# Kernel optimization log

Hardware: AMD Instinct MI355X
Metric: run time of the kernel (lower is better)

## Reference

```python
import jax, jax.numpy as jnp
import numpy as np

N, E, H = 40000, 640000, 128
EPS = 1e-5

def _bn(x, gamma, beta):
    # BatchNorm1d training-mode forward: batch mean / biased variance over axis 0
    mu = jnp.mean(x, axis=0)
    var = jnp.mean((x - mu) ** 2, axis=0)
    return (x - mu) * jax.lax.rsqrt(var + EPS) * gamma + beta


def setup_inputs() -> dict:
    key = jax.random.key(0)
    ks = jax.random.split(key, 12)
    s = 1.0 / np.sqrt(H)
    return {
        "x_feat": jax.random.normal(ks[0], (N, H), jnp.float32),
        "edge_attr": jax.random.normal(ks[1], (E, H), jnp.float32),
        "bases": jax.random.normal(ks[2], (E, H), jnp.float32),
        "src": jax.random.randint(ks[3], (E,), 0, N, jnp.int32),
        "dst": jax.random.randint(ks[4], (E,), 0, N, jnp.int32),
        "W1": jax.random.uniform(ks[5], (H, H), jnp.float32, -s, s),
        "b1": jnp.zeros((H,), jnp.float32),
        "W2": jax.random.uniform(ks[6], (H, H), jnp.float32, -s, s),
        "b2": jnp.zeros((H,), jnp.float32),
        "g1": jnp.ones((H,), jnp.float32),
        "be1": jnp.zeros((H,), jnp.float32),
        "W3": jax.random.uniform(ks[7], (H, H), jnp.float32, -s, s),
        "b3": jnp.zeros((H,), jnp.float32),
        "g2": jnp.ones((H,), jnp.float32),
        "be2": jnpp_zeros if False else jnp.zeros((H,), jnp.float32),
    }


def reference(x_feat, edge_attr, bases, src, dst,
              W1, b1, W2, b2, g1, be1, W3, b3, g2, be2):
    n_nodes = x_feat.shape[0]
    # edge gather-add: pos_e = x[src] + e
    pos_e = x_feat[src] + edge_attr                       # [E, H]
    # pre_ffn (Linear + exact GELU) then elementwise scale by bases
    v = jax.nn.gelu(pos_e @ W1.T + b1, approximate=False) * bases  # [E, H]
    # scatter-sum aggregation to destination nodes
    aggr = jax.ops.segment_sum(v, dst, num_segments=n_nodes)       # [N, H]
    # ffn: Linear -> BN -> GELU -> Linear -> BN -> GELU
    h = _bn(aggr @ W2.T + b2, g1, be1)
    h = jax.nn.gelu(h, approximate=False)
    h = _bn(h @ W3.T + b3, g2, be2)
    return jax.nn.gelu(h, approximate=False)
```

## Files before the change

### kernel.cpp

```cpp
#include <hip/hip_runtime.h>
#include <cmath>

#define H 128
#define EPS 1e-5f

typedef __attribute__((ext_vector_type(8))) __bf16 bf16x8;
typedef __attribute__((ext_vector_type(4))) float f32x4;
typedef __attribute__((ext_vector_type(2))) float f32x2;
typedef __attribute__((ext_vector_type(4))) unsigned short u16x4;
typedef __attribute__((ext_vector_type(8))) unsigned short u16x8;
typedef __attribute__((ext_vector_type(4))) int i32x4;

__device__ __forceinline__ float gelu_fast(float x) {
    float t2 = -1.5957691216057308f * fmaf(0.044715f * x * x, x, x);
    return x * __builtin_amdgcn_rcpf(1.0f + __expf(t2));
}

__device__ __forceinline__ unsigned short f2bfu(float f) {
    __bf16 h = (__bf16)f;
    return __builtin_bit_cast(unsigned short, h);
}

__device__ __forceinline__ float bfu2f(unsigned short u) {
    return __builtin_bit_cast(float, (unsigned)u << 16);
}

__device__ __forceinline__ void gld16(const void* g, void* l) {
    __builtin_amdgcn_global_load_lds(
        (__attribute__((address_space(1))) void*)(g),
        (__attribute__((address_space(3))) void*)(l), 16, 0, 0);
}

__global__ __launch_bounds__(256) void zero_kernel(int* __restrict__ p, int n4)
{
    int i = blockIdx.x * blockDim.x + threadIdx.x;
    const int stride = gridDim.x * blockDim.x;
    i32x4 z = {0, 0, 0, 0};
    for (; i < n4; i += stride)
        reinterpret_cast<i32x4*>(p)[i] = z;
}

__global__ __launch_bounds__(256) void hist_kernel(const int* __restrict__ dst,
                                                   int* __restrict__ cnt, int E)
{
    int i = blockIdx.x * blockDim.x + threadIdx.x;
    const int stride = gridDim.x * blockDim.x;
    for (; i < E; i += stride) atomicAdd(&cnt[dst[i]], 1);
}

__global__ __launch_bounds__(1024) void scan_kernel(const int* __restrict__ cnt,
                                                    int* __restrict__ offs,
                                                    int Nn, int E)
{
    __shared__ int part[1024];
    const int t = threadIdx.x;
    const int CH = (Nn + 1023) / 1024;
    const int base = t * CH;
    int s = 0;
    for (int i = 0; i < CH; ++i) {
        int idx = base + i;
        if (idx < Nn) s += cnt[idx];
    }
    part[t] = s;
    __syncthreads();
    for (int d = 1; d < 1024; d <<= 1) {
        int v = (t >= d) ? part[t - d] : 0;
        __syncthreads();
        part[t] += v;
        __syncthreads();
    }
    int run = (t > 0) ? part[t - 1] : 0;
    for (int i = 0; i < CH; ++i) {
        int idx = base + i;
        if (idx < Nn) {
            offs[idx] = run;
            run += cnt[idx];
        }
    }
    if (t == 0) offs[Nn] = E;
}

__global__ __launch_bounds__(256) void scatter_perm(const int* __restrict__ dst,
                                                    const int* __restrict__ offs,
                                                    int* __restrict__ cur2,
                                                    int* __restrict__ perm,
                                                    int* __restrict__ dsts, int E)
{
    int i = blockIdx.x * blockDim.x + threadIdx.x;
    const int stride = gridDim.x * blockDim.x;
    for (; i < E; i += stride) {
        int n = dst[i];
        int p = offs[n] + atomicAdd(&cur2[n], 1);
        perm[p] = i;
        dsts[p] = n;
    }
}

__global__ __launch_bounds__(256, 2) void edge_aggr(
    const float* __restrict__ x, const float* __restrict__ ea,
    const float* __restrict__ bases, const int* __restrict__ src,
    const int* __restrict__ perm, const int* __restrict__ dsts,
    const float* __restrict__ W1, const float* __restrict__ b1,
    float* __restrict__ aggr, int E)
{
    __shared__ __align__(16) float ealds[64 * 128];
    __shared__ __align__(16) float blds[64 * 128];
    __shared__ __align__(16) unsigned short xlds[64 * 128];

    const int tid = threadIdx.x;
    const int w = tid >> 6, l = tid & 63, lg = l >> 4, lr = l & 15;

    bf16x8 wf[2][4];
    f32x4 b1v[2];
#pragma unroll
    for (int ni = 0; ni < 2; ++ni) {
        int row = w * 32 + ni * 16 + lr;
#pragma unroll
        for (int kk = 0; kk < 4; ++kk) {
            const float* p = W1 + row * H + kk * 32 + lg * 8;
            u16x8 tt;
#pragma unroll
            for (int i = 0; i < 8; ++i) tt[i] = f2bfu(p[i]);
            wf[ni][kk] = __builtin_bit_cast(bf16x8, tt);
        }
        b1v[ni] = *reinterpret_cast<const f32x4*>(b1 + w * 32 + ni * 16 + lg * 4);
    }

    const int e0 = blockIdx.x * 64;
    int ic = e0 + l;
    ic = ic < E ? ic : E - 1;
    const int el_reg = perm[ic];
    const int nd_reg = dsts[ic];
    const int sr_reg = src[el_reg];

#pragma unroll
    for (int j = 0; j < 8; ++j) {
        const int r = (w << 4) + (j << 1) + (l >> 5);
        const int e = __shfl(el_reg, r);
        const int cs = (l & 31) ^ (r & 7);
        const int rowbase = (((w << 4) + (j << 1)) << 7);
        gld16(ea + (long)e * H + cs * 4, &ealds[rowbase]);
        gld16(bases + (long)e * H + cs * 4, &blds[rowbase]);
    }

#pragma unroll
    for (int it = 0; it < 8; ++it) {
        const int gch = it * 256 + tid;
        const int row = gch >> 5, c16 = gch & 31;
        const int s = __shfl(sr_reg, row);
        f32x4 b = *reinterpret_cast<const f32x4*>(x + (long)s * H + c16 * 4);
        u16x4 o;
#pragma unroll
        for (int j = 0; j < 4; ++j) o[j] = f2bfu(b[j]);
        const int scol = (c16 * 4) ^ ((row & 7) << 3);
        *reinterpret_cast<u16x4*>(&xlds[row * 128 + scol]) = o;
    }
    __syncthreads();

    const int col0base = w * 32 + lg * 4;
#pragma unroll
    for (int s = 0; s < 4; ++s) {
        const int arow = s * 16 + lr;
        const int fswz = arow & 7;
        const int xswz = fswz << 3;

        bf16x8 af[4];
#pragma unroll
        for (int kk = 0; kk < 4; ++kk) {
            const int cc = kk * 8 + lg * 2;
            f32x4 elo = *reinterpret_cast<const f32x4*>(&ealds[arow * 128 + ((cc ^ fswz) << 2)]);
            f32x4 ehi = *reinterpret_cast<const f32x4*>(&ealds[arow * 128 + (((cc + 1) ^ fswz) << 2)]);
            u16x8 xv = *reinterpret_cast<const u16x8*>(&xlds[arow * 128 + ((kk * 32 + lg * 8) ^ xswz)]);
            u16x8 o;
#pragma unroll
            for (int r = 0; r < 4; ++r) {
                o[r]     = f2bfu(elo[r] + bfu2f(xv[r]));
                o[r + 4] = f2bfu(ehi[r] + bfu2f(xv[r + 4]));
            }
            af[kk] = __builtin_bit_cast(bf16x8, o);
        }

        const int es = e0 + arow;
        const bool ok = es < E;
        const int nd = __shfl(nd_reg, arow);
        const int ndp = __shfl(nd_reg, arow - 1);
        const bool head = ok && (lr == 0 || nd != ndp);

#pragma unroll
        for (int ni = 0; ni < 2; ++ni) {
            f32x4 a4 = b1v[ni];
#pragma unroll
            for (int kk = 0; kk < 4; ++kk)
                a4 = __builtin_amdgcn_mfma_f32_16x16x32_bf16(wf[ni][kk], af[kk], a4, 0, 0, 0);

            const int col0 = col0base + ni * 16;
            const int bcc = col0 >> 2;
            f32x4 bq = *reinterpret_cast<const f32x4*>(&blds[arow * 128 + ((bcc ^ fswz) << 2)]);
            f32x4 v;
#pragma unroll
            for (int r = 0; r < 4; ++r)
                v[r] = ok ? gelu_fast(a4[r]) * bq[r] : 0.f;

#pragma unroll
            for (int d = 1; d < 16; d <<= 1) {
                f32x4 vn;
#pragma unroll
                for (int r = 0; r < 4; ++r) vn[r] = __shfl_down(v[r], d);
                int ndn = __shfl_down(nd, d);
                bool take = (lr + d < 16) && (ndn == nd);
#pragma unroll
                for (int r = 0; r < 4; ++r) v[r] += take ? vn[r] : 0.f;
            }

            if (head) {
                float* dstp = aggr + (long)nd * H + col0;
#pragma unroll
                for (int r = 0; r < 4; ++r) atomicAdd(&dstp[r], v[r]);
            }
        }
    }
}

template <bool PRE>
__global__ __launch_bounds__(256) void node_gemm(
    const float* __restrict__ A, const float* __restrict__ W,
    const float* __restrict__ bias, const float* __restrict__ scl,
    const float* __restrict__ shf, float* __restrict__ Y,
    float* __restrict__ csum, float* __restrict__ cssq, int Nn)
{
    __shared__ __align__(16) unsigned short alds[64 * 128];

    const int tid = threadIdx.x;
    const int w = tid >> 6, l = tid & 63, lg = l >> 4, lr = l & 15;
    const int er = tid >> 2, q = tid & 3;
    const int r0 = blockIdx.x * 64;

    bf16x8 bf[2][4];
    float bv[2];
#pragma unroll
    for (int n = 0; n < 2; ++n) {
        int row = w * 32 + n * 16 + lr;
        bv[n] = bias[row];
#pragma unroll
        for (int kk = 0; kk < 4; ++kk) {
            const float* p = W + row * H + kk * 32 + lg * 8;
            u16x8 t;
#pragma unroll
            for (int i = 0; i < 8; ++i) t[i] = f2bfu(p[i]);
            bf[n][kk] = __builtin_bit_cast(bf16x8, t);
        }
    }

    {
        int rr = r0 + er;
        int rc = rr < Nn ? rr : Nn - 1;
        const f32x4* pa = reinterpret_cast<const f32x4*>(A + (long)rc * H + q * 32);
        const int swz = (er & 7) << 3;
#pragma unroll
        for (int i = 0; i < 8; ++i) {
            f32x4 v = pa[i];
            if constexpr (PRE) {
                f32x4 sc = *reinterpret_cast<const f32x4*>(scl + q * 32 + i * 4);
                f32x4 sh = *reinterpret_cast<const f32x4*>(shf + q * 32 + i * 4);
#pragma unroll
                for (int c = 0; c < 4; ++c) v[c] = gelu_fast(v[c] * sc[c] + sh[c]);
            }
            u16x4 o;
            o[0] = f2bfu(v[0]);
            o[1] = f2bfu(v[1]);
            o[2] = f2bfu(v[2]);
            o[3] = f2bfu(v[3]);
            int col = q * 32 + i * 4;
            *reinterpret_cast<u16x4*>(&alds[er * 128 + (col ^ swz)]) = o;
        }
    }
    __syncthreads();

    float ps[2] = {0.f, 0.f}, ps2[2] = {0.f, 0.f};
#pragma unroll
    for (int m = 0; m < 4; ++m) {
        const int arow = m * 16 + lr;
        const int aswz = (arow & 7) << 3;
        bf16x8 af[4];
#pragma unroll
        for (int kk = 0; kk < 4; ++kk)
            af[kk] = __builtin_bit_cast(bf16x8,
                *reinterpret_cast<const u16x8*>(&alds[arow * 128 + ((kk * 32 + lg * 8) ^ aswz)]));
#pragma unroll
        for (int n = 0; n < 2; ++n) {
            f32x4 a4 = {0.f, 0.f, 0.f, 0.f};
#pragma unroll
            for (int kk = 0; kk < 4; ++kk)
                a4 = __builtin_amdgcn_mfma_f32_16x16x32_bf16(af[kk], bf[n][kk], a4, 0, 0, 0);
            const int j = w * 32 + n * 16 + lr;
#pragma unroll
            for (int r = 0; r < 4; ++r) {
                int rr = r0 + m * 16 + lg * 4 + r;
                if (rr < Nn) {
                    float z = a4[r] + bv[n];
                    Y[(long)rr * H + j] = z;
                    ps[n] += z;
                    ps2[n] += z * z;
                }
            }
        }
    }
#pragma unroll
    for (int n = 0; n < 2; ++n) {
        float s = ps[n];
        s += __shfl_xor(s, 16);
        s += __shfl_xor(s, 32);
        float s2 = ps2[n];
        s2 += __shfl_xor(s2, 16);
        s2 += __shfl_xor(s2, 32);
        if (lg == 0) {
            int j = w * 32 + n * 16 + lr;
            atomicAdd(&csum[j], s);
            atomicAdd(&cssq[j], s2);
        }
    }
}

__global__ void finalize_bn(const float* __restrict__ csum, const float* __restrict__ cssq,
                            const float* __restrict__ g, const float* __restrict__ be,
                            float* __restrict__ scl, float* __restrict__ shf, float invN)
{
    int j = threadIdx.x;
    float mu = csum[j] * invN;
    float var = fmaxf(cssq[j] * invN - mu * mu, 0.f);
    float s = g[j] * rsqrtf(var + EPS);
    scl[j] = s;
    shf[j] = be[j] - mu * s;
}

__global__ __launch_bounds__(256) void final_gelu(
    const float* __restrict__ Y2, const float* __restrict__ scl,
    const float* __restrict__ shf, float* __restrict__ out, long n4)
{
    long i = (long)blockIdx.x * blockDim.x + threadIdx.x;
    const long stride = (long)gridDim.x * blockDim.x;
    for (; i < n4; i += stride) {
        f32x4 v = reinterpret_cast<const f32x4*>(Y2)[i];
        int c4 = (int)(i & 31);
        f32x4 sc = reinterpret_cast<const f32x4*>(scl)[c4];
        f32x4 sh = reinterpret_cast<const f32x4*>(shf)[c4];
        f32x4 o;
#pragma unroll
        for (int c = 0; c < 4; ++c) o[c] = gelu_fast(v[c] * sc[c] + sh[c]);
        reinterpret_cast<f32x4*>(out)[i] = o;
    }
}

extern "C" void kernel_launch(void* const* d_in, const int* in_sizes, int n_in,
                              void* d_out, int out_size, void* d_ws, size_t ws_size,
                              hipStream_t stream) {
    const float* x     = (const float*)d_in[0];
    const float* ea    = (const float*)d_in[1];
    const float* bases = (const float*)d_in[2];
    const int*   src   = (const int*)d_in[3];
    const int*   dst   = (const int*)d_in[4];
    const float* W1    = (const float*)d_in[5];
    const float* b1    = (const float*)d_in[6];
    const float* W2    = (const float*)d_in[7];
    const float* b2    = (const float*)d_in[8];
    const float* g1    = (const float*)d_in[9];
    const float* be1   = (const float*)d_in[10];
    const float* W3    = (const float*)d_in[11];
    const float* b3    = (const float*)d_in[12];
    const float* g2    = (const float*)d_in[13];
    const float* be2   = (const float*)d_in[14];

    const int N = in_sizes[0] / H;
    const int E = in_sizes[1] / H;

    float* ws    = (float*)d_ws;
    float* aggr  = ws;
    float* y1    = aggr + (size_t)N * H;
    float* stats = y1 + (size_t)N * H;
    float* sum1 = stats,        *ss1 = stats + 128;
    float* sum2 = stats + 256,  *ss2 = stats + 384;
    float* scl1 = stats + 512,  *shf1 = stats + 640;
    float* scl2 = stats + 768,  *shf2 = stats + 896;
    int* cnt  = (int*)(stats + 1024);
    int* cnt2 = cnt + N;
    int* perm = cnt2 + N;
    int* dsts = perm + E;
    int* offs = dsts + E;

    const int zn4 = (1024 + 2 * N + 3) / 4;
    zero_kernel<<<128, 256, 0, stream>>>((int*)stats, zn4);
    zero_kernel<<<1024, 256, 0, stream>>>((int*)aggr, N * H / 4);

    hist_kernel<<<2048, 256, 0, stream>>>(dst, cnt, E);
    scan_kernel<<<1, 1024, 0, stream>>>(cnt, offs, N, E);
    scatter_perm<<<2048, 256, 0, stream>>>(dst, offs, cnt2, perm, dsts, E);

    edge_aggr<<<(E + 63) / 64, 256, 0, stream>>>(x, ea, bases, src, perm, dsts,
                                                 W1, b1, aggr, E);

    const int nblk = (N + 63) / 64;
    node_gemm<false><<<nblk, 256, 0, stream>>>(aggr, W2, b2, nullptr, nullptr, y1, sum1, ss1, N);
    finalize_bn<<<1, 128, 0, stream>>>(sum1, ss1, g1, be1, scl1, shf1, 1.0f / (float)N);
    node_gemm<true><<<nblk, 256, 0, stream>>>(y1, W3, b3, scl1, shf1, aggr, sum2, ss2, N);
    finalize_bn<<<1, 128, 0, stream>>>(sum2, ss2, g2, be2, scl2, shf2, 1.0f / (float)N);

    long n4 = (long)N * H / 4;
    final_gelu<<<2048, 256, 0, stream>>>(aggr, scl2, shf2, (float*)d_out, n4);
}
```

Measured before the change: 463.3 us.

## Pre-convert x to bf16 for async LDS gathers and parallelize the offset scan

Adds a pass that converts x to bf16 once, so the edge kernel gathers x[src] rows with direct global-to-LDS loads. This halves the gathered bytes and removes the per-edge conversion and register staging. The single-block serial scan is also replaced with a three-kernel multi-block scan, cutting serial latency in the CSR build. The cost is an extra pass over x, extra workspace, and two more kernel launches.

```diff
diff --git a/kernel.cpp b/kernel.cpp
--- a/kernel.cpp
+++ b/kernel.cpp
@@ -40,6 +40,22 @@
         reinterpret_cast<i32x4*>(p)[i] = z;
 }
 
+__global__ __launch_bounds__(256) void convert_x(const float* __restrict__ x,
+                                                 unsigned short* __restrict__ xb,
+                                                 long n8)
+{
+    long i = (long)blockIdx.x * blockDim.x + threadIdx.x;
+    const long stride = (long)gridDim.x * blockDim.x;
+    for (; i < n8; i += stride) {
+        f32x4 a = *reinterpret_cast<const f32x4*>(x + i * 8);
+        f32x4 b = *reinterpret_cast<const f32x4*>(x + i * 8 + 4);
+        u16x8 o;
+#pragma unroll
+        for (int j = 0; j < 4; ++j) { o[j] = f2bfu(a[j]); o[j + 4] = f2bfu(b[j]); }
+        *reinterpret_cast<u16x8*>(xb + i * 8) = o;
+    }
+}
+
 __global__ __launch_bounds__(256) void hist_kernel(const int* __restrict__ dst,
                                                    int* __restrict__ cnt, int E)
 {
@@ -48,36 +64,51 @@
     for (; i < E; i += stride) atomicAdd(&cnt[dst[i]], 1);
 }
 
-__global__ __launch_bounds__(1024) void scan_kernel(const int* __restrict__ cnt,
-                                                    int* __restrict__ offs,
-                                                    int Nn, int E)
-{
-    __shared__ int part[1024];
+__global__ __launch_bounds__(256) void scan_p1(const int* __restrict__ cnt,
+                                               int* __restrict__ otmp,
+                                               int* __restrict__ bsum, int Nn)
+{
+    __shared__ int sh[256];
     const int t = threadIdx.x;
-    const int CH = (Nn + 1023) / 1024;
-    const int base = t * CH;
-    int s = 0;
-    for (int i = 0; i < CH; ++i) {
-        int idx = base + i;
-        if (idx < Nn) s += cnt[idx];
-    }
-    part[t] = s;
+    const int idx = blockIdx.x * 256 + t;
+    int v = idx < Nn ? cnt[idx] : 0;
+    sh[t] = v;
     __syncthreads();
-    for (int d = 1; d < 1024; d <<= 1) {
-        int v = (t >= d) ? part[t - d] : 0;
+    for (int d = 1; d < 256; d <<= 1) {
+        int u = (t >= d) ? sh[t - d] : 0;
         __syncthreads();
-        part[t] += v;
+        sh[t] += u;
         __syncthreads();
     }
-    int run = (t > 0) ? part[t - 1] : 0;
-    for (int i = 0; i < CH; ++i) {
-        int idx = base + i;
-        if (idx < Nn) {
-            offs[idx] = run;
-            run += cnt[idx];
-        }
-    }
+    if (idx < Nn) otmp[idx] = sh[t] - v;
+    if (t == 255) bsum[blockIdx.x] = sh[t];
+}
+
+__global__ __launch_bounds__(256) void scan_p2(const int* __restrict__ bsum,
+                                               int* __restrict__ boff, int nb,
+                                               int* __restrict__ offs, int Nn, int E)
+{
+    __shared__ int sh[256];
+    const int t = threadIdx.x;
+    int v = t < nb ? bsum[t] : 0;
+    sh[t] = v;
+    __syncthreads();
+    for (int d = 1; d < 256; d <<= 1) {
+        int u = (t >= d) ? sh[t - d] : 0;
+        __syncthreads();
+        sh[t] += u;
+        __syncthreads();
+    }
+    if (t < nb) boff[t] = sh[t] - v;
     if (t == 0) offs[Nn] = E;
+}
+
+__global__ __launch_bounds__(256) void scan_p3(const int* __restrict__ otmp,
+                                               const int* __restrict__ boff,
+                                               int* __restrict__ offs, int Nn)
+{
+    const int idx = blockIdx.x * 256 + threadIdx.x;
+    if (idx < Nn) offs[idx] = otmp[idx] + boff[blockIdx.x];
 }
 
 __global__ __launch_bounds__(256) void scatter_perm(const int* __restrict__ dst,
@@ -97,7 +128,7 @@
 }
 
 __global__ __launch_bounds__(256, 2) void edge_aggr(
-    const float* __restrict__ x, const float* __restrict__ ea,
+    const unsigned short* __restrict__ xbf, const float* __restrict__ ea,
     const float* __restrict__ bases, const int* __restrict__ src,
     const int* __restrict__ perm, const int* __restrict__ dsts,
     const float* __restrict__ W1, const float* __restrict__ b1,
@@ -144,16 +175,12 @@
     }
 
 #pragma unroll
-    for (int it = 0; it < 8; ++it) {
-        const int gch = it * 256 + tid;
-        const int row = gch >> 5, c16 = gch & 31;
-        const int s = __shfl(sr_reg, row);
-        f32x4 b = *reinterpret_cast<const f32x4*>(x + (long)s * H + c16 * 4);
-        u16x4 o;
-#pragma unroll
-        for (int j = 0; j < 4; ++j) o[j] = f2bfu(b[j]);
-        const int scol = (c16 * 4) ^ ((row & 7) << 3);
-        *reinterpret_cast<u16x4*>(&xlds[row * 128 + scol]) = o;
+    for (int j = 0; j < 4; ++j) {
+        const int r = (w << 4) + (j << 2) + (l >> 4);
+        const int s = __shfl(sr_reg, r);
+        const int cs = (l & 15) ^ (r & 7);
+        const int rowbase = (((w << 4) + (j << 2)) << 7);
+        gld16(xbf + (long)s * H + cs * 8, &xlds[rowbase]);
     }
     __syncthreads();
 
@@ -162,7 +189,6 @@
     for (int s = 0; s < 4; ++s) {
         const int arow = s * 16 + lr;
         const int fswz = arow & 7;
-        const int xswz = fswz << 3;
 
         bf16x8 af[4];
 #pragma unroll
@@ -170,7 +196,7 @@
             const int cc = kk * 8 + lg * 2;
             f32x4 elo = *reinterpret_cast<const f32x4*>(&ealds[arow * 128 + ((cc ^ fswz) << 2)]);
             f32x4 ehi = *reinterpret_cast<const f32x4*>(&ealds[arow * 128 + (((cc + 1) ^ fswz) << 2)]);
-            u16x8 xv = *reinterpret_cast<const u16x8*>(&xlds[arow * 128 + ((kk * 32 + lg * 8) ^ xswz)]);
+            u16x8 xv = *reinterpret_cast<const u16x8*>(&xlds[arow * 128 + (((kk * 4 + lg) ^ fswz) << 3)]);
             u16x8 o;
 #pragma unroll
             for (int r = 0; r < 4; ++r) {
@@ -386,16 +412,25 @@
     int* perm = cnt2 + N;
     int* dsts = perm + E;
     int* offs = dsts + E;
+    int* otmp = offs + N + 1;
+    int* bsum = otmp + N;
+    int* boff = bsum + 256;
+    unsigned short* xbf = (unsigned short*)(((uintptr_t)(boff + 256) + 4095) & ~(uintptr_t)4095);
 
     const int zn4 = (1024 + 2 * N + 3) / 4;
     zero_kernel<<<128, 256, 0, stream>>>((int*)stats, zn4);
     zero_kernel<<<1024, 256, 0, stream>>>((int*)aggr, N * H / 4);
 
+    convert_x<<<2048, 256, 0, stream>>>(x, xbf, (long)N * H / 8);
+
+    const int nsb = (N + 255) / 256;
     hist_kernel<<<2048, 256, 0, stream>>>(dst, cnt, E);
-    scan_kernel<<<1, 1024, 0, stream>>>(cnt, offs, N, E);
+    scan_p1<<<nsb, 256, 0, stream>>>(cnt, otmp, bsum, N);
+    scan_p2<<<1, 256, 0, stream>>>(bsum, boff, nsb, offs, N, E);
+    scan_p3<<<nsb, 256, 0, stream>>>(otmp, boff, offs, N);
     scatter_perm<<<2048, 256, 0, stream>>>(dst, offs, cnt2, perm, dsts, E);
 
-    edge_aggr<<<(E + 63) / 64, 256, 0, stream>>>(x, ea, bases, src, perm, dsts,
+    edge_aggr<<<(E + 63) / 64, 256, 0, stream>>>(xbf, ea, bases, src, perm, dsts,
                                                  W1, b1, aggr, E);
 
     const int nblk = (N + 63) / 64;
```

Result: faster. 393.6 us (-15.0%).
